# Optimization experiments

Hardware: AMD Instinct MI355X
Metric: run time of the kernel (lower is better)

The kernel has to match this reference:

```python
import jax, jax.numpy as jnp
import numpy as np


def setup_inputs() -> dict:
    key = jax.random.key(0)
    k1, k2 = jax.random.split(key)
    B, T, D = 8, 2048, 2048
    layer_in = jax.random.normal(k1, (B, T, D), dtype=jnp.float32)
    # nn.Linear(2D, 2D): weight [out=2D, in=2D], bias [2D]
    W_gate = jax.random.normal(k2, (2 * D, 2 * D), dtype=jnp.float32) * 0.02
    b_gate = jnp.zeros((2 * D,), dtype=jnp.float32)
    return {"layer_in": layer_in, "W_gate": W_gate, "b_gate": b_gate}


def reference(layer_in, W_gate, b_gate):
    # Cumulative average: tril(ones)/row_index @ x  ==  cumsum(x)/[1..t]
    t = layer_in.shape[1]
    denom = jnp.arange(1, t + 1, dtype=layer_in.dtype)[:, None]  # (t, 1)
    average_out = jnp.cumsum(layer_in, axis=1) / denom  # (B, t, D)
    # Gating: Linear(2D -> 2D) on concat(x, avg), then chunk into two gates
    gating_in = jnp.concatenate([layer_in, average_out], axis=-1)  # (B, t, 2D)
    gates = jnp.einsum('btk,ok->bto', gating_in, W_gate) + b_gate  # (B, t, 2D)
    input_gate, forget_gate = jnp.split(gates, 2, axis=2)
    gating_out = (jax.nn.sigmoid(input_gate) * layer_in
                  + jax.nn.sigmoid(forget_gate) * average_out)
    return gating_out, average_out
```

## Files before the change

kernel.cpp:

```cpp
#include <hip/hip_runtime.h>
#include <hip/hip_bf16.h>


#define Bb 8
#define Tt 2048
#define Dd 2048
#define Mm (Bb * Tt)
#define Kk 4096
#define NC 32
#define CT 64

typedef __bf16 bf16x8 __attribute__((ext_vector_type(8)));
typedef float f32x4 __attribute__((ext_vector_type(4)));

__device__ __forceinline__ void gload16(const void* g, void* l) {
    __builtin_amdgcn_global_load_lds(
        (const __attribute__((address_space(1))) unsigned int*)g,
        (__attribute__((address_space(3))) unsigned int*)l, 16, 0, 0);
}

__global__ void wconv_kernel(const float* __restrict__ W,
                             unsigned short* __restrict__ Wb, long n) {
    long i = ((long)blockIdx.x * blockDim.x + threadIdx.x) * 4;
    long stride = (long)gridDim.x * blockDim.x * 4;
    for (; i < n; i += stride) {
        float4 v = *(const float4*)(W + i);
        __hip_bfloat16 a = __float2bfloat16(v.x);
        __hip_bfloat16 b = __float2bfloat16(v.y);
        __hip_bfloat16 c = __float2bfloat16(v.z);
        __hip_bfloat16 d = __float2bfloat16(v.w);
        ushort4 u;
        u.x = *(unsigned short*)&a; u.y = *(unsigned short*)&b;
        u.z = *(unsigned short*)&c; u.w = *(unsigned short*)&d;
        *(ushort4*)(Wb + i) = u;
    }
}

__global__ void ksum_kernel(const float* __restrict__ X, float* __restrict__ S,
                            unsigned short* __restrict__ Gin) {
    int d = blockIdx.y * 256 + threadIdx.x;
    int bc = blockIdx.x;
    int b = bc >> 5, c = bc & 31;
    const float* p = X + ((long)(b * Tt + c * CT)) * Dd + d;
    long row = (long)b * Tt + c * CT;
    float s = 0.f;
#pragma unroll 8
    for (int t = 0; t < CT; ++t) {
        float x = p[(long)t * Dd];
        s += x;
        __hip_bfloat16 xb = __float2bfloat16(x);
        Gin[(row + t) * 4096 + d] = *(unsigned short*)&xb;
    }
    S[(long)bc * Dd + d] = s;
}

__global__ void kscan_kernel(const unsigned short* __restrict__ Ginx,
                             const float* __restrict__ S,
                             float* __restrict__ AVG, unsigned short* __restrict__ Gin) {
    int d = blockIdx.y * 256 + threadIdx.x;
    int bc = blockIdx.x;
    int b = bc >> 5, c = bc & 31;
    const float* Sp = S + (long)(b * NC) * Dd + d;
    float run = 0.f;
    for (int cc = 0; cc < c; ++cc) run += Sp[(long)cc * Dd];
    long row = (long)b * Tt + c * CT;
    for (int tt = 0; tt < CT; ++tt) {
        long r = row + tt;
        union { unsigned int u; float f; } cx;
        cx.u = ((unsigned int)Ginx[r * 4096 + d]) << 16;
        run += cx.f;
        float av = run / (float)(c * CT + tt + 1);
        AVG[r * Dd + d] = av;
        __hip_bfloat16 ab = __float2bfloat16(av);
        Gin[r * 4096 + 2048 + d] = *(unsigned short*)&ab;
    }
}

#define MFMA(va, vb, c_) c_ = __builtin_amdgcn_mfma_f32_16x16x32_bf16(va, vb, c_, 0, 0, 0)
#define RD(p_, i_) (*(const bf16x8*)((p_) + (i_) * 1024))
#define SBAR __builtin_amdgcn_s_barrier()
#define SCHB __builtin_amdgcn_sched_barrier(0)
#define LGKM0 do { asm volatile("s_waitcnt lgkmcnt(0)" ::: "memory"); SCHB; } while (0)

#define CL_LO(B0_, B1_, B2_, B3_)                                               \
    __builtin_amdgcn_s_setprio(1);                                              \
    MFMA(aL0,B0_,acc[0][0]); MFMA(aL0,B1_,acc[0][1]); MFMA(aL0,B2_,acc[0][2]); MFMA(aL0,B3_,acc[0][3]); \
    MFMA(aL1,B0_,acc[1][0]); MFMA(aL1,B1_,acc[1][1]); MFMA(aL1,B2_,acc[1][2]); MFMA(aL1,B3_,acc[1][3]); \
    MFMA(aL2,B0_,acc[2][0]); MFMA(aL2,B1_,acc[2][1]); MFMA(aL2,B2_,acc[2][2]); MFMA(aL2,B3_,acc[2][3]); \
    MFMA(aL3,B0_,acc[3][0]); MFMA(aL3,B1_,acc[3][1]); MFMA(aL3,B2_,acc[3][2]); MFMA(aL3,B3_,acc[3][3]); \
    __builtin_amdgcn_s_setprio(0);
#define CL_HI(B0_, B1_, B2_, B3_)                                               \
    __builtin_amdgcn_s_setprio(1);                                              \
    MFMA(aH0,B0_,acc[4][0]); MFMA(aH0,B1_,acc[4][1]); MFMA(aH0,B2_,acc[4][2]); MFMA(aH0,B3_,acc[4][3]); \
    MFMA(aH1,B0_,acc[5][0]); MFMA(aH1,B1_,acc[5][1]); MFMA(aH1,B2_,acc[5][2]); MFMA(aH1,B3_,acc[5][3]); \
    MFMA(aH2,B0_,acc[6][0]); MFMA(aH2,B1_,acc[6][1]); MFMA(aH2,B2_,acc[6][2]); MFMA(aH2,B3_,acc[6][3]); \
    MFMA(aH3,B0_,acc[7][0]); MFMA(aH3,B1_,acc[7][1]); MFMA(aH3,B2_,acc[7][2]); MFMA(aH3,B3_,acc[7][3]); \
    __builtin_amdgcn_s_setprio(0);

#define SLOT(sOFF_, snOFF_, stOFF_, t4_, B0_,B1_,B2_,B3_, N0_,N1_,N2_,N3_, STG_, RDX_, VN_) \
  {                                                                             \
    const char* pa_ = rA0 + (sOFF_);                                            \
    const char* qa_ = rA0 + (snOFF_);                                           \
    const char* qb_ = rB0 + (snOFF_);                                           \
    char* st_ = ldsb + (stOFF_) + woff;                                         \
    const long ko_ = (long)(t4_) * 64;                                          \
    LGKM0;                                          \
    aH0 = RD(pa_,4); aH1 = RD(pa_,5); aH2 = RD(pa_,6); aH3 = RD(pa_,7);         \
    if (STG_) { gload16(gA0 + ko_, st_); gload16(gA1 + ko_, st_ + 8192); }      \
    SCHB;                                                                       \
    CL_LO(B0_, B1_, B2_, B3_)                                                   \
    SCHB;                                                                       \
    LGKM0;                                                      \
    if (RDX_) {                                                                 \
      aL0 = RD(qa_,0); aL1 = RD(qa_,1); aL2 = RD(qa_,2); aL3 = RD(qa_,3);       \
      N0_ = RD(qb_,0); N1_ = RD(qb_,1); N2_ = RD(qb_,2); N3_ = RD(qb_,3);       \
    }                                                                           \
    if (STG_) { gload16(gB0 + ko_, st_ + 16384); gload16(gB1 + ko_, st_ + 24576); } \
    SCHB;                                                                       \
    CL_HI(B0_, B1_, B2_, B3_)                                                   \
    SCHB;                                                                       \
    asm volatile("s_waitcnt vmcnt(" #VN_ ")" ::: "memory");                     \
    SBAR; SCHB;                                                                 \
  }

#define S0 0
#define S1 32768
#define S2 65536
#define S3 98304
#define S4 131072

__global__ __launch_bounds__(512, 1) void gemm5r_kernel(
    const unsigned short* __restrict__ Gin,
    const unsigned short* __restrict__ Wb,
    const float* __restrict__ bias,
    float* __restrict__ OUT)
{
    __shared__ __attribute__((aligned(128))) char lds[163840];
    char* ldsb = (char*)lds;

    const int tid = threadIdx.x;
    const int w = tid >> 6, l = tid & 63;
    const int wm = w >> 2, wn = w & 3;
    const int lm = l & 15;
    const int woff = w * 1024;

    const int bid = blockIdx.x;
    const int batch = bid >> 8;
    const int rr = bid & 255;
    const int xcd = rr & 7;
    const int j = rr >> 3;
    const int nt = xcd * 2 + (j >> 4);
    const int mt = batch * 16 + (j & 15);
    const long m0 = (long)mt * 256;
    const int n0 = nt * 128;

    const int srow = tid >> 2;
    const int schunk = (tid & 3) ^ ((tid >> 3) & 3);
    const char* gA0 = (const char*)Gin + (m0 + srow) * 8192 + schunk * 16;
    const char* gA1 = gA0 + 128 * 8192;
    const long jr0 = n0 + ((srow >> 6) << 5) + (srow & 31) + (((srow >> 5) & 1) << 11);
    const int j1 = 128 + srow;
    const long jr1 = n0 + ((j1 >> 6) << 5) + (j1 & 31) + (((j1 >> 5) & 1) << 11);
    const char* gB0 = (const char*)Wb + jr0 * 8192 + schunk * 16;
    const char* gB1 = (const char*)Wb + jr1 * 8192 + schunk * 16;

    const int cbyte = (((l >> 4) ^ ((lm >> 1) & 3))) * 16;
    const char* rA0 = ldsb + (wm * 128 + lm) * 64 + cbyte;
    const char* rB0 = ldsb + 16384 + (wn * 64 + lm) * 64 + cbyte;

    f32x4 acc[8][4] = {};

    bf16x8 aL0, aL1, aL2, aL3, aH0, aH1, aH2, aH3;
    bf16x8 bb0, bb1, bb2, bb3, bd0, bd1, bd2, bd3;

    gload16(gA0,       ldsb + S0 + woff);
    gload16(gA1,       ldsb + S0 + 8192 + woff);
    gload16(gB0,       ldsb + S0 + 16384 + woff);
    gload16(gB1,       ldsb + S0 + 24576 + woff);
    gload16(gA0 + 64,  ldsb + S1 + woff);
    gload16(gA1 + 64,  ldsb + S1 + 8192 + woff);
    gload16(gB0 + 64,  ldsb + S1 + 16384 + woff);
    gload16(gB1 + 64,  ldsb + S1 + 24576 + woff);
    gload16(gA0 + 128, ldsb + S2 + woff);
    gload16(gA1 + 128, ldsb + S2 + 8192 + woff);
    gload16(gB0 + 128, ldsb + S2 + 16384 + woff);
    gload16(gB1 + 128, ldsb + S2 + 24576 + woff);
    gload16(gA0 + 192, ldsb + S3 + woff);
    gload16(gA1 + 192, ldsb + S3 + 8192 + woff);
    gload16(gB0 + 192, ldsb + S3 + 16384 + woff);
    gload16(gB1 + 192, ldsb + S3 + 24576 + woff);
    asm volatile("s_waitcnt vmcnt(8)" ::: "memory");
    SBAR; SCHB;
    aL0 = RD(rA0,0); aL1 = RD(rA0,1); aL2 = RD(rA0,2); aL3 = RD(rA0,3);
    bb0 = RD(rB0,0); bb1 = RD(rB0,1); bb2 = RD(rB0,2); bb3 = RD(rB0,3);
    SCHB;

#pragma unroll 1
    for (int t = 0; t < 120; t += 10) {
        SLOT(S0,S1,S4, t+4,  bb0,bb1,bb2,bb3, bd0,bd1,bd2,bd3, 1,1,8)
        SLOT(S1,S2,S0, t+5,  bd0,bd1,bd2,bd3, bb0,bb1,bb2,bb3, 1,1,8)
        SLOT(S2,S3,S1, t+6,  bb0,bb1,bb2,bb3, bd0,bd1,bd2,bd3, 1,1,8)
        SLOT(S3,S4,S2, t+7,  bd0,bd1,bd2,bd3, bb0,bb1,bb2,bb3, 1,1,8)
        SLOT(S4,S0,S3, t+8,  bb0,bb1,bb2,bb3, bd0,bd1,bd2,bd3, 1,1,8)
        SLOT(S0,S1,S4, t+9,  bd0,bd1,bd2,bd3, bb0,bb1,bb2,bb3, 1,1,8)
        SLOT(S1,S2,S0, t+10, bb0,bb1,bb2,bb3, bd0,bd1,bd2,bd3, 1,1,8)
        SLOT(S2,S3,S1, t+11, bd0,bd1,bd2,bd3, bb0,bb1,bb2,bb3, 1,1,8)
        SLOT(S3,S4,S2, t+12, bb0,bb1,bb2,bb3, bd0,bd1,bd2,bd3, 1,1,8)
        SLOT(S4,S0,S3, t+13, bd0,bd1,bd2,bd3, bb0,bb1,bb2,bb3, 1,1,8)
    }
    SLOT(S0,S1,S4, 124, bb0,bb1,bb2,bb3, bd0,bd1,bd2,bd3, 1,1,8)
    SLOT(S1,S2,S0, 125, bd0,bd1,bd2,bd3, bb0,bb1,bb2,bb3, 1,1,8)
    SLOT(S2,S3,S1, 126, bb0,bb1,bb2,bb3, bd0,bd1,bd2,bd3, 1,1,8)
    SLOT(S3,S4,S2, 127, bd0,bd1,bd2,bd3, bb0,bb1,bb2,bb3, 1,1,8)
    SLOT(S4,S0,S3, 0,   bb0,bb1,bb2,bb3, bd0,bd1,bd2,bd3, 0,1,4)
    SLOT(S0,S1,S4, 0,   bd0,bd1,bd2,bd3, bb0,bb1,bb2,bb3, 0,1,0)
    SLOT(S1,S2,S0, 0,   bb0,bb1,bb2,bb3, bd0,bd1,bd2,bd3, 0,1,0)
    SLOT(S2,S3,S1, 0,   bd0,bd1,bd2,bd3, bb0,bb1,bb2,bb3, 0,0,0)

#pragma unroll
    for (int mi = 0; mi < 8; ++mi) {
        long rbase = m0 + wm * 128 + mi * 16 + (l >> 4) * 4;
#pragma unroll
        for (int nj = 0; nj < 2; ++nj) {
            int d = n0 + wn * 32 + nj * 16 + lm;
            float bi_ = bias[d];
            float bf_ = bias[d + 2048];
#pragma unroll
            for (int r = 0; r < 4; ++r) {
                long row = rbase + r;
                unsigned int ux = Gin[row * 4096 + d];
                unsigned int ua = Gin[row * 4096 + 2048 + d];
                union { unsigned int u; float f; } cx, ca;
                cx.u = ux << 16; ca.u = ua << 16;
                float gi = acc[mi][nj][r] + bi_;
                float gf = acc[mi][nj + 2][r] + bf_;
                float si = 1.f / (1.f + __expf(-gi));
                float sf = 1.f / (1.f + __expf(-gf));
                OUT[row * 2048 + d] = si * cx.f + sf * ca.f;
            }
        }
    }
}

extern "C" void kernel_launch(void* const* d_in, const int* in_sizes, int n_in,
                              void* d_out, int out_size, void* d_ws, size_t ws_size,
                              hipStream_t stream) {
    const float* X = (const float*)d_in[0];
    const float* W = (const float*)d_in[1];
    const float* bias = (const float*)d_in[2];

    float* OUT = (float*)d_out;
    float* AVG = OUT + (long)Mm * Dd;

    char* ws = (char*)d_ws;
    unsigned short* Wb  = (unsigned short*)ws;
    unsigned short* Gin = (unsigned short*)(ws + 33554432);
    float* S = (float*)(ws + 33554432 + 134217728);

    wconv_kernel<<<2048, 256, 0, stream>>>(W, Wb, (long)Kk * Kk);
    ksum_kernel<<<dim3(Bb * NC, Dd / 256), 256, 0, stream>>>(X, S, Gin);
    kscan_kernel<<<dim3(Bb * NC, Dd / 256), 256, 0, stream>>>(Gin, S, AVG, Gin);
    gemm5r_kernel<<<1024, 512, 0, stream>>>(Gin, Wb, bias, OUT);
}
```

Before: 594.6 us.

## Switch GEMM to 32x32x16 MFMA with matching LDS swizzle and epilogue

Replaces the 16x16x32 bf16 MFMA tiling with 32x32x16 MFMA, so each wave issues 8 larger MFMAs per half-step instead of 16 small ones. It reloads fewer B fragments per step, changes the LDS swizzle and the W row mapping for staging, and rewrites the epilogue for the 16-element accumulator layout. The goal is fewer LDS reads and better MFMA throughput per instruction. The risk is bank conflicts from the new swizzle and a less favourable epilogue store pattern.

```diff
diff --git a/kernel.cpp b/kernel.cpp
--- a/kernel.cpp
+++ b/kernel.cpp
@@ -11,7 +11,7 @@
 #define CT 64
 
 typedef __bf16 bf16x8 __attribute__((ext_vector_type(8)));
-typedef float f32x4 __attribute__((ext_vector_type(4)));
+typedef float f32x16 __attribute__((ext_vector_type(16)));
 
 __device__ __forceinline__ void gload16(const void* g, void* l) {
     __builtin_amdgcn_global_load_lds(
@@ -76,48 +76,53 @@
     }
 }
 
-#define MFMA(va, vb, c_) c_ = __builtin_amdgcn_mfma_f32_16x16x32_bf16(va, vb, c_, 0, 0, 0)
-#define RD(p_, i_) (*(const bf16x8*)((p_) + (i_) * 1024))
+#define MFMA32(va, vb, c_) c_ = __builtin_amdgcn_mfma_f32_32x32x16_bf16(va, vb, c_, 0, 0, 0)
 #define SBAR __builtin_amdgcn_s_barrier()
 #define SCHB __builtin_amdgcn_sched_barrier(0)
 #define LGKM0 do { asm volatile("s_waitcnt lgkmcnt(0)" ::: "memory"); SCHB; } while (0)
 
-#define CL_LO(B0_, B1_, B2_, B3_)                                               \
+#define CL0_                                                                    \
     __builtin_amdgcn_s_setprio(1);                                              \
-    MFMA(aL0,B0_,acc[0][0]); MFMA(aL0,B1_,acc[0][1]); MFMA(aL0,B2_,acc[0][2]); MFMA(aL0,B3_,acc[0][3]); \
-    MFMA(aL1,B0_,acc[1][0]); MFMA(aL1,B1_,acc[1][1]); MFMA(aL1,B2_,acc[1][2]); MFMA(aL1,B3_,acc[1][3]); \
-    MFMA(aL2,B0_,acc[2][0]); MFMA(aL2,B1_,acc[2][1]); MFMA(aL2,B2_,acc[2][2]); MFMA(aL2,B3_,acc[2][3]); \
-    MFMA(aL3,B0_,acc[3][0]); MFMA(aL3,B1_,acc[3][1]); MFMA(aL3,B2_,acc[3][2]); MFMA(aL3,B3_,acc[3][3]); \
+    MFMA32(aL0, bL0, acc[0][0]); MFMA32(aL0, bL1, acc[0][1]);                   \
+    MFMA32(aL1, bL0, acc[1][0]); MFMA32(aL1, bL1, acc[1][1]);                   \
+    MFMA32(aL2, bL0, acc[2][0]); MFMA32(aL2, bL1, acc[2][1]);                   \
+    MFMA32(aL3, bL0, acc[3][0]); MFMA32(aL3, bL1, acc[3][1]);                   \
     __builtin_amdgcn_s_setprio(0);
-#define CL_HI(B0_, B1_, B2_, B3_)                                               \
+#define CL1_                                                                    \
     __builtin_amdgcn_s_setprio(1);                                              \
-    MFMA(aH0,B0_,acc[4][0]); MFMA(aH0,B1_,acc[4][1]); MFMA(aH0,B2_,acc[4][2]); MFMA(aH0,B3_,acc[4][3]); \
-    MFMA(aH1,B0_,acc[5][0]); MFMA(aH1,B1_,acc[5][1]); MFMA(aH1,B2_,acc[5][2]); MFMA(aH1,B3_,acc[5][3]); \
-    MFMA(aH2,B0_,acc[6][0]); MFMA(aH2,B1_,acc[6][1]); MFMA(aH2,B2_,acc[6][2]); MFMA(aH2,B3_,acc[6][3]); \
-    MFMA(aH3,B0_,acc[7][0]); MFMA(aH3,B1_,acc[7][1]); MFMA(aH3,B2_,acc[7][2]); MFMA(aH3,B3_,acc[7][3]); \
+    MFMA32(aH0, bH0, acc[0][0]); MFMA32(aH0, bH1, acc[0][1]);                   \
+    MFMA32(aH1, bH0, acc[1][0]); MFMA32(aH1, bH1, acc[1][1]);                   \
+    MFMA32(aH2, bH0, acc[2][0]); MFMA32(aH2, bH1, acc[2][1]);                   \
+    MFMA32(aH3, bH0, acc[3][0]); MFMA32(aH3, bH1, acc[3][1]);                   \
     __builtin_amdgcn_s_setprio(0);
 
-#define SLOT(sOFF_, snOFF_, stOFF_, t4_, B0_,B1_,B2_,B3_, N0_,N1_,N2_,N3_, STG_, RDX_, VN_) \
+#define SLOT(sOFF_, snOFF_, stOFF_, t4_, STG_, RDX_, VN_)                       \
   {                                                                             \
-    const char* pa_ = rA0 + (sOFF_);                                            \
-    const char* qa_ = rA0 + (snOFF_);                                           \
-    const char* qb_ = rB0 + (snOFF_);                                           \
+    const char* p0_ = rAk1 + (sOFF_);                                           \
+    const char* p1_ = rBk1 + (sOFF_);                                           \
+    const char* q0_ = rAk0 + (snOFF_);                                          \
+    const char* q1_ = rBk0 + (snOFF_);                                          \
     char* st_ = ldsb + (stOFF_) + woff;                                         \
     const long ko_ = (long)(t4_) * 64;                                          \
-    LGKM0;                                          \
-    aH0 = RD(pa_,4); aH1 = RD(pa_,5); aH2 = RD(pa_,6); aH3 = RD(pa_,7);         \
+    LGKM0;                                        \
+                                 \
+    aH0 = *(const bf16x8*)(p0_);        aH1 = *(const bf16x8*)(p0_ + 2048);     \
+    aH2 = *(const bf16x8*)(p0_ + 4096); aH3 = *(const bf16x8*)(p0_ + 6144);     \
+    bH0 = *(const bf16x8*)(p1_);        bH1 = *(const bf16x8*)(p1_ + 8192);     \
     if (STG_) { gload16(gA0 + ko_, st_); gload16(gA1 + ko_, st_ + 8192); }      \
     SCHB;                                                                       \
-    CL_LO(B0_, B1_, B2_, B3_)                                                   \
-    SCHB;                                                                       \
-    LGKM0;                                                      \
+    CL0_                                                                        \
+    SCHB;                                                                       \
+    LGKM0;                                                         \
+                           \
     if (RDX_) {                                                                 \
-      aL0 = RD(qa_,0); aL1 = RD(qa_,1); aL2 = RD(qa_,2); aL3 = RD(qa_,3);       \
-      N0_ = RD(qb_,0); N1_ = RD(qb_,1); N2_ = RD(qb_,2); N3_ = RD(qb_,3);       \
+      aL0 = *(const bf16x8*)(q0_);        aL1 = *(const bf16x8*)(q0_ + 2048);   \
+      aL2 = *(const bf16x8*)(q0_ + 4096); aL3 = *(const bf16x8*)(q0_ + 6144);   \
+      bL0 = *(const bf16x8*)(q1_);        bL1 = *(const bf16x8*)(q1_ + 8192);   \
     }                                                                           \
     if (STG_) { gload16(gB0 + ko_, st_ + 16384); gload16(gB1 + ko_, st_ + 24576); } \
     SCHB;                                                                       \
-    CL_HI(B0_, B1_, B2_, B3_)                                                   \
+    CL1_                                                                        \
     SCHB;                                                                       \
     asm volatile("s_waitcnt vmcnt(" #VN_ ")" ::: "memory");                     \
     SBAR; SCHB;                                                                 \
@@ -129,7 +134,7 @@
 #define S3 98304
 #define S4 131072
 
-__global__ __launch_bounds__(512, 1) void gemm5r_kernel(
+__global__ __launch_bounds__(512, 1) void gemm5r32_kernel(
     const unsigned short* __restrict__ Gin,
     const unsigned short* __restrict__ Wb,
     const float* __restrict__ bias,
@@ -141,7 +146,8 @@
     const int tid = threadIdx.x;
     const int w = tid >> 6, l = tid & 63;
     const int wm = w >> 2, wn = w & 3;
-    const int lm = l & 15;
+    const int la = l & 31;
+    const int lk = l >> 5;
     const int woff = w * 1024;
 
     const int bid = blockIdx.x;
@@ -155,23 +161,23 @@
     const int n0 = nt * 128;
 
     const int srow = tid >> 2;
-    const int schunk = (tid & 3) ^ ((tid >> 3) & 3);
+    const int schunk = (tid & 3) ^ ((tid >> 2) & 3);
     const char* gA0 = (const char*)Gin + (m0 + srow) * 8192 + schunk * 16;
     const char* gA1 = gA0 + 128 * 8192;
-    const long jr0 = n0 + ((srow >> 6) << 5) + (srow & 31) + (((srow >> 5) & 1) << 11);
-    const int j1 = 128 + srow;
-    const long jr1 = n0 + ((j1 >> 6) << 5) + (j1 & 31) + (((j1 >> 5) & 1) << 11);
-    const char* gB0 = (const char*)Wb + jr0 * 8192 + schunk * 16;
-    const char* gB1 = (const char*)Wb + jr1 * 8192 + schunk * 16;
-
-    const int cbyte = (((l >> 4) ^ ((lm >> 1) & 3))) * 16;
-    const char* rA0 = ldsb + (wm * 128 + lm) * 64 + cbyte;
-    const char* rB0 = ldsb + 16384 + (wn * 64 + lm) * 64 + cbyte;
-
-    f32x4 acc[8][4] = {};
-
-    bf16x8 aL0, aL1, aL2, aL3, aH0, aH1, aH2, aH3;
-    bf16x8 bb0, bb1, bb2, bb3, bd0, bd1, bd2, bd3;
+    const char* gB0 = (const char*)Wb + ((long)(n0 + srow)) * 8192 + schunk * 16;
+    const char* gB1 = (const char*)Wb + ((long)(2048 + n0 + srow)) * 8192 + schunk * 16;
+
+    const int cb0 = (lk ^ (la & 3)) * 16;
+    const int cb1 = ((2 + lk) ^ (la & 3)) * 16;
+    const char* rAk0 = ldsb + wm * 8192 + la * 64 + cb0;
+    const char* rAk1 = ldsb + wm * 8192 + la * 64 + cb1;
+    const char* rBk0 = ldsb + 16384 + (wn * 32 + la) * 64 + cb0;
+    const char* rBk1 = ldsb + 16384 + (wn * 32 + la) * 64 + cb1;
+
+    f32x16 acc[4][2] = {};
+
+    bf16x8 aL0, aL1, aL2, aL3, bL0, bL1;
+    bf16x8 aH0, aH1, aH2, aH3, bH0, bH1;
 
     gload16(gA0,       ldsb + S0 + woff);
     gload16(gA1,       ldsb + S0 + 8192 + woff);
@@ -191,53 +197,53 @@
     gload16(gB1 + 192, ldsb + S3 + 24576 + woff);
     asm volatile("s_waitcnt vmcnt(8)" ::: "memory");
     SBAR; SCHB;
-    aL0 = RD(rA0,0); aL1 = RD(rA0,1); aL2 = RD(rA0,2); aL3 = RD(rA0,3);
-    bb0 = RD(rB0,0); bb1 = RD(rB0,1); bb2 = RD(rB0,2); bb3 = RD(rB0,3);
+    aL0 = *(const bf16x8*)(rAk0);        aL1 = *(const bf16x8*)(rAk0 + 2048);
+    aL2 = *(const bf16x8*)(rAk0 + 4096); aL3 = *(const bf16x8*)(rAk0 + 6144);
+    bL0 = *(const bf16x8*)(rBk0);        bL1 = *(const bf16x8*)(rBk0 + 8192);
     SCHB;
 
 #pragma unroll 1
     for (int t = 0; t < 120; t += 10) {
-        SLOT(S0,S1,S4, t+4,  bb0,bb1,bb2,bb3, bd0,bd1,bd2,bd3, 1,1,8)
-        SLOT(S1,S2,S0, t+5,  bd0,bd1,bd2,bd3, bb0,bb1,bb2,bb3, 1,1,8)
-        SLOT(S2,S3,S1, t+6,  bb0,bb1,bb2,bb3, bd0,bd1,bd2,bd3, 1,1,8)
-        SLOT(S3,S4,S2, t+7,  bd0,bd1,bd2,bd3, bb0,bb1,bb2,bb3, 1,1,8)
-        SLOT(S4,S0,S3, t+8,  bb0,bb1,bb2,bb3, bd0,bd1,bd2,bd3, 1,1,8)
-        SLOT(S0,S1,S4, t+9,  bd0,bd1,bd2,bd3, bb0,bb1,bb2,bb3, 1,1,8)
-        SLOT(S1,S2,S0, t+10, bb0,bb1,bb2,bb3, bd0,bd1,bd2,bd3, 1,1,8)
-        SLOT(S2,S3,S1, t+11, bd0,bd1,bd2,bd3, bb0,bb1,bb2,bb3, 1,1,8)
-        SLOT(S3,S4,S2, t+12, bb0,bb1,bb2,bb3, bd0,bd1,bd2,bd3, 1,1,8)
-        SLOT(S4,S0,S3, t+13, bd0,bd1,bd2,bd3, bb0,bb1,bb2,bb3, 1,1,8)
-    }
-    SLOT(S0,S1,S4, 124, bb0,bb1,bb2,bb3, bd0,bd1,bd2,bd3, 1,1,8)
-    SLOT(S1,S2,S0, 125, bd0,bd1,bd2,bd3, bb0,bb1,bb2,bb3, 1,1,8)
-    SLOT(S2,S3,S1, 126, bb0,bb1,bb2,bb3, bd0,bd1,bd2,bd3, 1,1,8)
-    SLOT(S3,S4,S2, 127, bd0,bd1,bd2,bd3, bb0,bb1,bb2,bb3, 1,1,8)
-    SLOT(S4,S0,S3, 0,   bb0,bb1,bb2,bb3, bd0,bd1,bd2,bd3, 0,1,4)
-    SLOT(S0,S1,S4, 0,   bd0,bd1,bd2,bd3, bb0,bb1,bb2,bb3, 0,1,0)
-    SLOT(S1,S2,S0, 0,   bb0,bb1,bb2,bb3, bd0,bd1,bd2,bd3, 0,1,0)
-    SLOT(S2,S3,S1, 0,   bd0,bd1,bd2,bd3, bb0,bb1,bb2,bb3, 0,0,0)
-
+        SLOT(S0,S1,S4, t+4,  1,1,8)
+        SLOT(S1,S2,S0, t+5,  1,1,8)
+        SLOT(S2,S3,S1, t+6,  1,1,8)
+        SLOT(S3,S4,S2, t+7,  1,1,8)
+        SLOT(S4,S0,S3, t+8,  1,1,8)
+        SLOT(S0,S1,S4, t+9,  1,1,8)
+        SLOT(S1,S2,S0, t+10, 1,1,8)
+        SLOT(S2,S3,S1, t+11, 1,1,8)
+        SLOT(S3,S4,S2, t+12, 1,1,8)
+        SLOT(S4,S0,S3, t+13, 1,1,8)
+    }
+    SLOT(S0,S1,S4, 124, 1,1,8)
+    SLOT(S1,S2,S0, 125, 1,1,8)
+    SLOT(S2,S3,S1, 126, 1,1,8)
+    SLOT(S3,S4,S2, 127, 1,1,8)
+    SLOT(S4,S0,S3, 0,   0,1,4)
+    SLOT(S0,S1,S4, 0,   0,1,0)
+    SLOT(S1,S2,S0, 0,   0,1,0)
+    SLOT(S2,S3,S1, 0,   0,0,0)
+
+    const int d = n0 + wn * 32 + la;
+    const float bi_ = bias[d];
+    const float bf_ = bias[d + 2048];
 #pragma unroll
-    for (int mi = 0; mi < 8; ++mi) {
-        long rbase = m0 + wm * 128 + mi * 16 + (l >> 4) * 4;
+    for (int mi = 0; mi < 4; ++mi) {
+        const long rb = m0 + wm * 128 + mi * 32 + lk * 4;
+        f32x16 ci = acc[mi][0];
+        f32x16 cf = acc[mi][1];
 #pragma unroll
-        for (int nj = 0; nj < 2; ++nj) {
-            int d = n0 + wn * 32 + nj * 16 + lm;
-            float bi_ = bias[d];
-            float bf_ = bias[d + 2048];
-#pragma unroll
-            for (int r = 0; r < 4; ++r) {
-                long row = rbase + r;
-                unsigned int ux = Gin[row * 4096 + d];
-                unsigned int ua = Gin[row * 4096 + 2048 + d];
-                union { unsigned int u; float f; } cx, ca;
-                cx.u = ux << 16; ca.u = ua << 16;
-                float gi = acc[mi][nj][r] + bi_;
-                float gf = acc[mi][nj + 2][r] + bf_;
-                float si = 1.f / (1.f + __expf(-gi));
-                float sf = 1.f / (1.f + __expf(-gf));
-                OUT[row * 2048 + d] = si * cx.f + sf * ca.f;
-            }
+        for (int qq = 0; qq < 16; ++qq) {
+            long row = rb + (qq & 3) + 8 * (qq >> 2);
+            unsigned int ux = Gin[row * 4096 + d];
+            unsigned int ua = Gin[row * 4096 + 2048 + d];
+            union { unsigned int u; float f; } cx, ca;
+            cx.u = ux << 16; ca.u = ua << 16;
+            float gi = ci[qq] + bi_;
+            float gf = cf[qq] + bf_;
+            float si = 1.f / (1.f + __expf(-gi));
+            float sf = 1.f / (1.f + __expf(-gf));
+            OUT[row * 2048 + d] = si * cx.f + sf * ca.f;
         }
     }
 }
@@ -260,5 +266,5 @@
     wconv_kernel<<<2048, 256, 0, stream>>>(W, Wb, (long)Kk * Kk);
     ksum_kernel<<<dim3(Bb * NC, Dd / 256), 256, 0, stream>>>(X, S, Gin);
     kscan_kernel<<<dim3(Bb * NC, Dd / 256), 256, 0, stream>>>(Gin, S, AVG, Gin);
-    gemm5r_kernel<<<1024, 512, 0, stream>>>(Gin, Wb, bias, OUT);
-}
+    gemm5r32_kernel<<<1024, 512, 0, stream>>>(Gin, Wb, bias, OUT);
+}
```

Result: slower. 663.4 us (+11.6%).
